# Performance work log

Measured on AMD Instinct MI355X. Metric: run time of the kernel, lower is better.

Reference implementation:

```python
import jax, jax.numpy as jnp
import numpy as np

K_STEPS = 10
ALPHA = 0.1


def setup_inputs() -> dict:
    key = jax.random.key(0)
    k0, k1, k2, k3 = jax.random.split(key, 4)
    N, E, C_IN, C_HID, C_OUT = 100000, 3200000, 512, 256, 64
    x = jax.random.normal(k0, (N, C_IN), dtype=jnp.float32)
    edge_index = jax.random.randint(k1, (2, E), 0, N, dtype=jnp.int64)
    W1 = jax.random.normal(k2, (C_IN, C_HID), dtype=jnp.float32) * (1.0 / np.sqrt(C_IN))
    b1 = jnp.zeros((C_HID,), dtype=jnp.float32)
    W2 = jax.random.normal(k3, (C_HID, C_OUT), dtype=jnp.float32) * (1.0 / np.sqrt(C_HID))
    b2 = jnp.zeros((C_OUT,), dtype=jnp.float32)
    return {"x": x, "edge_index": edge_index, "W1": W1, "b1": b1, "W2": W2, "b2": b2}


def reference(x, edge_index, W1, b1, W2, b2):
    N = x.shape[0]
    src, dst = edge_index[0], edge_index[1]
    # add self-loops (PyG APPNP default)
    loop = jnp.arange(N, dtype=src.dtype)
    src = jnp.concatenate([src, loop])
    dst = jnp.concatenate([dst, loop])
    # GCN symmetric normalization: D^{-1/2} A D^{-1/2}
    deg = jax.ops.segment_sum(jnp.ones_like(dst, dtype=x.dtype), dst, num_segments=N)
    dinv = jnp.where(deg > 0, deg ** -0.5, jnp.zeros_like(deg))
    norm = dinv[src] * dinv[dst]  # [E+N]
    # MLP (dropout is identity at inference)
    h = jax.nn.relu(x @ W1 + b1) @ W2 + b2  # [N, C_OUT]
    # K-step APPNP propagation with teleport
    out = h
    for _ in range(K_STEPS):
        msg = norm[:, None] * out[src]  # [E+N, C_OUT]
        agg = jax.ops.segment_sum(msg, dst, num_segments=N)
        out = (1.0 - ALPHA) * agg + ALPHA * h
    return jax.nn.log_softmax(out, axis=1)
```

## Files before the change

### kernel.cpp

```cpp
#include <hip/hip_runtime.h>
#include <hip/hip_bf16.h>

#define C_IN  512
#define C_HID 256
#define C_OUT 64
#define K_STEPS 10
#define ALPHA 0.1f

#define BKT_SHIFT 9
#define BKT_NODES 512
#define BCAP 24576
#define EPB 4096

typedef _Float16 half8 __attribute__((ext_vector_type(8)));
typedef float f32x4 __attribute__((ext_vector_type(4)));


__global__ __launch_bounds__(256) void k_bucketA(
    const int* __restrict__ src, const int* __restrict__ dst, int E,
    int* __restrict__ bcursor, long long* __restrict__ bedges, int nbkt)
{
    __shared__ int lcount[256];
    __shared__ int lbase[256];
    int t = threadIdx.x;
    int base = blockIdx.x * EPB;
    for (int i = t; i < nbkt; i += 256) lcount[i] = 0;
    __syncthreads();

    int       mybkt[16];
    int       myoff[16];
    long long mypk[16];
    #pragma unroll
    for (int j = 0; j < 16; j++) {
        int e = base + j * 256 + t;
        if (e < E) {
            int s = src[e], d = dst[e];
            int b = d >> BKT_SHIFT;
            mybkt[j] = b;
            mypk[j]  = ((long long)d << 32) | (unsigned int)s;
            myoff[j] = atomicAdd(&lcount[b], 1);
        } else {
            mybkt[j] = -1;
        }
    }
    __syncthreads();
    for (int i = t; i < nbkt; i += 256)
        lbase[i] = lcount[i] ? atomicAdd(&bcursor[i], lcount[i]) : 0;
    __syncthreads();
    #pragma unroll
    for (int j = 0; j < 16; j++) {
        if (mybkt[j] >= 0) {
            int p = lbase[mybkt[j]] + myoff[j];
            bedges[(size_t)mybkt[j] * BCAP + p] = mypk[j];
        }
    }
}

__global__ __launch_bounds__(256) void k_bcount(
    const int* __restrict__ bcursor, const long long* __restrict__ bedges,
    int* __restrict__ counts, int N)
{
    __shared__ int lcnt[BKT_NODES];
    int b = blockIdx.x, t = threadIdx.x;
    int nodebase = b << BKT_SHIFT;
    for (int i = t; i < BKT_NODES; i += 256) lcnt[i] = 0;
    __syncthreads();
    int cnt = bcursor[b];
    const long long* be = bedges + (size_t)b * BCAP;
    for (int i = t; i < cnt; i += 256) {
        int d = (int)(be[i] >> 32);
        atomicAdd(&lcnt[d - nodebase], 1);
    }
    __syncthreads();
    for (int i = t; i < BKT_NODES; i += 256) {
        int node = nodebase + i;
        if (node < N) counts[node] = lcnt[i];
    }
}

__global__ __launch_bounds__(256) void k_bscatter(
    const int* __restrict__ bcursor, const long long* __restrict__ bedges,
    const int* __restrict__ rowptr, int* __restrict__ csr_src, int N)
{
    __shared__ int lcur[BKT_NODES];
    int b = blockIdx.x, t = threadIdx.x;
    int nodebase = b << BKT_SHIFT;
    for (int i = t; i < BKT_NODES; i += 256) {
        int node = nodebase + i;
        lcur[i] = (node < N) ? rowptr[node] : 0;
    }
    __syncthreads();
    int cnt = bcursor[b];
    const long long* be = bedges + (size_t)b * BCAP;
    for (int i = t; i < cnt; i += 256) {
        long long pk = be[i];
        int d = (int)(pk >> 32);
        int s = (int)pk;
        int p = atomicAdd(&lcur[d - nodebase], 1);
        csr_src[p] = s;
    }
}


__global__ void k_dinv(const int* __restrict__ counts, float* __restrict__ dinv, int N) {
    int i = blockIdx.x * blockDim.x + threadIdx.x;
    if (i < N) {
        float deg = (float)(counts[i] + 1);
        dinv[i] = 1.0f / sqrtf(deg);
    }
}

#define SCAN_CHUNK 2048

__global__ void k_scan1(const int* __restrict__ counts, int N, int* __restrict__ bsum) {
    __shared__ int sdata[256];
    int b = blockIdx.x, t = threadIdx.x;
    int base = b * SCAN_CHUNK;
    int sum = 0;
    for (int i = t; i < SCAN_CHUNK; i += 256) {
        int idx = base + i;
        sum += (idx < N) ? counts[idx] : 0;
    }
    sdata[t] = sum;
    __syncthreads();
    for (int off = 128; off; off >>= 1) {
        if (t < off) sdata[t] += sdata[t + off];
        __syncthreads();
    }
    if (t == 0) bsum[b] = sdata[0];
}

__global__ void k_scan2(int* __restrict__ bsum, int nb, int E, int* __restrict__ rowptr, int N) {
    if (blockIdx.x == 0 && threadIdx.x == 0) {
        int run = 0;
        for (int i = 0; i < nb; i++) { int v = bsum[i]; bsum[i] = run; run += v; }
        rowptr[N] = E;
    }
}

__global__ void k_scan3(const int* __restrict__ counts, int N,
                        const int* __restrict__ bsum, int* __restrict__ rowptr) {
    __shared__ int sdata[256];
    int b = blockIdx.x, t = threadIdx.x;
    int base = b * SCAN_CHUNK;
    int vals[8];
    int local = 0;
    #pragma unroll
    for (int i = 0; i < 8; i++) {
        int idx = base + t * 8 + i;
        vals[i] = (idx < N) ? counts[idx] : 0;
        local += vals[i];
    }
    sdata[t] = local;
    __syncthreads();
    for (int off = 1; off < 256; off <<= 1) {
        int y = 0;
        if (t >= off) y = sdata[t - off];
        __syncthreads();
        sdata[t] += y;
        __syncthreads();
    }
    int excl = (t == 0) ? 0 : sdata[t - 1];
    int run = bsum[b] + excl;
    #pragma unroll
    for (int i = 0; i < 8; i++) {
        int idx = base + t * 8 + i;
        if (idx < N) rowptr[idx] = run;
        run += vals[i];
    }
}


__global__ void k_w1t(const float* __restrict__ W, _Float16* __restrict__ Wt) {
    int i = blockIdx.x * 256 + threadIdx.x;
    int k = i >> 8, n = i & 255;
    Wt[(size_t)n * 512 + k] = (_Float16)W[i];
}

__global__ void k_w2t(const float* __restrict__ W, _Float16* __restrict__ Wt) {
    int i = blockIdx.x * 256 + threadIdx.x;
    int k = i >> 6, n = i & 63;
    Wt[(size_t)n * 256 + k] = (_Float16)W[i];
}


__global__ __launch_bounds__(256, 2) void k_mlp1(
    const float* __restrict__ A, const _Float16* __restrict__ Bt,
    const float* __restrict__ bias, _Float16* __restrict__ C, int M)
{
    __shared__ float lds[3][128 * 32];

    int t    = threadIdx.x;
    int lane = t & 63;
    int wid  = t >> 6;
    int bm   = blockIdx.x * 128;
    int wr   = wid >> 1;
    int wc   = wid & 1;
    int mrow = lane & 15;
    int kg   = lane >> 4;

    int srow = wid * 8 + (lane >> 3);
    int cgs  = (lane & 7) ^ (lane >> 3);

    const float* gsrc[4];
    #pragma unroll
    for (int q = 0; q < 4; q++) {
        int gr = bm + q * 32 + srow;
        if (gr >= M) gr = M - 1;
        gsrc[q] = A + (size_t)gr * 512 + cgs * 4;
    }

    #define STAGE(buf, ks)                                                       \
        {                                                                        \
            _Pragma("unroll")                                                    \
            for (int q = 0; q < 4; q++) {                                        \
                __builtin_amdgcn_global_load_lds(                                \
                    (const __attribute__((address_space(1))) void*)(gsrc[q] + (ks) * 32), \
                    (__attribute__((address_space(3))) void*)((char*)&lds[buf][0] + q * 4096 + wid * 1024), \
                    16, 0, 0);                                                   \
            }                                                                    \
        }

    f32x4 acc[4][8] = {};

    int m7 = lane & 7;
    int rbase[4];
    #pragma unroll
    for (int mi = 0; mi < 4; mi++)
        rbase[mi] = (wr * 64 + mi * 16 + mrow) * 32;
    int p0 = ((2 * kg) ^ m7) * 4;
    int p1 = ((2 * kg + 1) ^ m7) * 4;

    STAGE(0, 0);
    STAGE(1, 1);

    #pragma unroll
    for (int ks = 0; ks < 16; ks++) {
        asm volatile("s_waitcnt vmcnt(4) lgkmcnt(0)" ::: "memory");
        __builtin_amdgcn_s_barrier();

        half8 b[8];
        #pragma unroll
        for (int ni = 0; ni < 8; ni++) {
            int n = wc * 128 + ni * 16 + mrow;
            b[ni] = *(const half8*)(Bt + (size_t)n * 512 + ks * 32 + kg * 8);
        }

        if (ks < 14) STAGE((ks + 2) % 3, ks + 2);

        const float* lbuf = &lds[ks % 3][0];

        half8 a[4];
        #pragma unroll
        for (int mi = 0; mi < 4; mi++) {
            f32x4 lo = *(const f32x4*)&lbuf[rbase[mi] + p0];
            f32x4 hi = *(const f32x4*)&lbuf[rbase[mi] + p1];
            a[mi][0] = (_Float16)lo[0]; a[mi][1] = (_Float16)lo[1];
            a[mi][2] = (_Float16)lo[2]; a[mi][3] = (_Float16)lo[3];
            a[mi][4] = (_Float16)hi[0]; a[mi][5] = (_Float16)hi[1];
            a[mi][6] = (_Float16)hi[2]; a[mi][7] = (_Float16)hi[3];
        }

        #pragma unroll
        for (int mi = 0; mi < 4; mi++)
            #pragma unroll
            for (int ni = 0; ni < 8; ni++)
                acc[mi][ni] = __builtin_amdgcn_mfma_f32_16x16x32_f16(
                    a[mi], b[ni], acc[mi][ni], 0, 0, 0);
    }
    #undef STAGE

    #pragma unroll
    for (int mi = 0; mi < 4; mi++) {
        #pragma unroll
        for (int ni = 0; ni < 8; ni++) {
            int n = wc * 128 + ni * 16 + mrow;
            float bv = bias[n];
            #pragma unroll
            for (int rg = 0; rg < 4; rg++) {
                int row = bm + wr * 64 + mi * 16 + kg * 4 + rg;
                if (row < M) {
                    float v = acc[mi][ni][rg] + bv;
                    C[(size_t)row * 256 + n] = (_Float16)fmaxf(v, 0.f);
                }
            }
        }
    }
}


__global__ __launch_bounds__(256) void k_mlp2(
    const _Float16* __restrict__ A, const _Float16* __restrict__ Bt,
    const float* __restrict__ bias, const float* __restrict__ dinv,
    _Float16* __restrict__ C, _Float16* __restrict__ Y, int M)
{
    int lane = threadIdx.x & 63;
    int wid  = threadIdx.x >> 6;
    int bm   = blockIdx.x * 256 + wid * 64;
    int mrow = lane & 15;
    int kg   = lane >> 4;
    f32x4 acc[4][4] = {};

    int r[4];
    #pragma unroll
    for (int mi = 0; mi < 4; mi++) {
        int rr = bm + mi * 16 + mrow;
        r[mi] = rr < M ? rr : M - 1;
    }

    for (int k0 = 0; k0 < 256; k0 += 32) {
        int k = k0 + kg * 8;
        half8 a[4], b[4];
        #pragma unroll
        for (int mi = 0; mi < 4; mi++)
            a[mi] = *(const half8*)(A + (size_t)r[mi] * 256 + k);
        #pragma unroll
        for (int ni = 0; ni < 4; ni++) {
            int n = ni * 16 + mrow;
            b[ni] = *(const half8*)(Bt + (size_t)n * 256 + k);
        }
        #pragma unroll
        for (int mi = 0; mi < 4; mi++)
            #pragma unroll
            for (int ni = 0; ni < 4; ni++)
                acc[mi][ni] = __builtin_amdgcn_mfma_f32_16x16x32_f16(
                    a[mi], b[ni], acc[mi][ni], 0, 0, 0);
    }

    #pragma unroll
    for (int mi = 0; mi < 4; mi++) {
        #pragma unroll
        for (int ni = 0; ni < 4; ni++) {
            int n = ni * 16 + mrow;
            float bv = bias[n];
            #pragma unroll
            for (int rg = 0; rg < 4; rg++) {
                int row = bm + mi * 16 + kg * 4 + rg;
                if (row < M) {
                    float v = acc[mi][ni][rg] + bv;
                    C[(size_t)row * 64 + n] = (_Float16)v;
                    Y[(size_t)row * 64 + n] = (_Float16)(v * dinv[row]);
                }
            }
        }
    }
}


template <bool LAST>
__global__ __launch_bounds__(256) void k_prop(
    const int* __restrict__ rowptr, const int* __restrict__ csr_src,
    const float* __restrict__ dinv, const _Float16* __restrict__ h,
    const _Float16* __restrict__ ycur, _Float16* __restrict__ ynxt,
    float* __restrict__ out, int N)
{
    int node = blockIdx.x * 4 + (threadIdx.x >> 6);
    if (node >= N) return;
    int lane = threadIdx.x & 63;
    int g  = lane >> 3;
    int cg = lane & 7;

    int beg = rowptr[node], end = rowptr[node + 1];
    float dn = dinv[node];
    half8 ys = *(const half8*)(ycur + ((size_t)node << 6) + cg * 8);
    half8 hv = *(const half8*)(h    + ((size_t)node << 6) + cg * 8);

    float acc[8] = {};
    for (int e = beg + g; e < end; e += 32) {
        int i1 = e + 8, i2 = e + 16, i3 = e + 24;
        float p1 = (i1 < end) ? 1.f : 0.f;
        float p2 = (i2 < end) ? 1.f : 0.f;
        float p3 = (i3 < end) ? 1.f : 0.f;
        int s0 = csr_src[e];
        int s1 = csr_src[(i1 < end) ? i1 : e];
        int s2 = csr_src[(i2 < end) ? i2 : e];
        int s3 = csr_src[(i3 < end) ? i3 : e];
        half8 v0 = *(const half8*)(ycur + ((size_t)s0 << 6) + cg * 8);
        half8 v1 = *(const half8*)(ycur + ((size_t)s1 << 6) + cg * 8);
        half8 v2 = *(const half8*)(ycur + ((size_t)s2 << 6) + cg * 8);
        half8 v3 = *(const half8*)(ycur + ((size_t)s3 << 6) + cg * 8);
        #pragma unroll
        for (int c = 0; c < 8; c++)
            acc[c] += ((float)v0[c] + p1 * (float)v1[c])
                    + (p2 * (float)v2[c] + p3 * (float)v3[c]);
    }

    #pragma unroll
    for (int c = 0; c < 8; c++) {
        float a = acc[c];
        a += __shfl_xor(a, 8);
        a += __shfl_xor(a, 16);
        a += __shfl_xor(a, 32);
        acc[c] = a;
    }

    float o[8];
    #pragma unroll
    for (int c = 0; c < 8; c++)
        o[c] = (1.0f - ALPHA) * dn * (acc[c] + (float)ys[c]) + ALPHA * (float)hv[c];

    if (!LAST) {
        if (g == 0) {
            half8 w;
            #pragma unroll
            for (int c = 0; c < 8; c++) w[c] = (_Float16)(dn * o[c]);
            *(half8*)(ynxt + ((size_t)node << 6) + cg * 8) = w;
        }
    } else {
        float m = o[0];
        #pragma unroll
        for (int c = 1; c < 8; c++) m = fmaxf(m, o[c]);
        m = fmaxf(m, __shfl_xor(m, 1));
        m = fmaxf(m, __shfl_xor(m, 2));
        m = fmaxf(m, __shfl_xor(m, 4));
        float s = 0.f;
        #pragma unroll
        for (int c = 0; c < 8; c++) s += __expf(o[c] - m);
        s += __shfl_xor(s, 1);
        s += __shfl_xor(s, 2);
        s += __shfl_xor(s, 4);
        float ls = m + logf(s);
        if (g == 0) {
            f32x4 w0, w1;
            #pragma unroll
            for (int c = 0; c < 4; c++) { w0[c] = o[c] - ls; w1[c] = o[c + 4] - ls; }
            float* p = out + ((size_t)node << 6) + cg * 8;
            *(f32x4*)p = w0;
            *(f32x4*)(p + 4) = w1;
        }
    }
}


extern "C" void kernel_launch(void* const* d_in, const int* in_sizes, int n_in,
                              void* d_out, int out_size, void* d_ws, size_t ws_size,
                              hipStream_t stream) {
    const float* x  = (const float*)d_in[0];
    const int*   ei = (const int*)d_in[1];
    const float* W1 = (const float*)d_in[2];
    const float* b1 = (const float*)d_in[3];
    const float* W2 = (const float*)d_in[4];
    const float* b2 = (const float*)d_in[5];

    const int N = in_sizes[0] / C_IN;
    const int E = in_sizes[1] / 2;
    const int* src = ei;
    const int* dst = ei + E;

    char* ws = (char*)d_ws;
    size_t off = 0;
    auto alloc = [&](size_t bytes) -> void* {
        void* p = ws + off;
        off += (bytes + 255) & ~(size_t)255;
        return p;
    };

    int nb   = (N + SCAN_CHUNK - 1) / SCAN_CHUNK;
    int nbkt = (N + BKT_NODES - 1) / BKT_NODES;

    int*       counts  = (int*)      alloc((size_t)4 * N);
    int*       rowptr  = (int*)      alloc((size_t)4 * (N + 1));
    float*     dinv    = (float*)    alloc((size_t)4 * N);
    int*       bsum    = (int*)      alloc((size_t)4 * (nb + 1));
    int*       bcursor = (int*)      alloc((size_t)4 * nbkt);
    int*       csr_src = (int*)      alloc((size_t)4 * E);
    _Float16*  W1t     = (_Float16*) alloc((size_t)2 * C_IN * C_HID);
    _Float16*  W2t     = (_Float16*) alloc((size_t)2 * C_HID * C_OUT);
    _Float16*  hmid    = (_Float16*) alloc((size_t)2 * N * C_HID);
    _Float16*  h       = (_Float16*) alloc((size_t)2 * N * C_OUT);
    _Float16*  ybuf0   = (_Float16*) alloc((size_t)2 * N * C_OUT);
    _Float16*  ybuf1   = (_Float16*) alloc((size_t)2 * N * C_OUT);
    _Float16*  ybuf2   = (_Float16*) alloc((size_t)2 * N * C_OUT);

    long long* bedges = (long long*)hmid;

    hipMemsetAsync(bcursor, 0, (size_t)4 * nbkt, stream);
    k_bucketA<<<(E + EPB - 1) / EPB, 256, 0, stream>>>(src, dst, E, bcursor, bedges, nbkt);
    k_bcount<<<nbkt, 256, 0, stream>>>(bcursor, bedges, counts, N);
    k_dinv<<<(N + 255) / 256, 256, 0, stream>>>(counts, dinv, N);
    k_scan1<<<nb, 256, 0, stream>>>(counts, N, bsum);
    k_scan2<<<1, 64, 0, stream>>>(bsum, nb, E, rowptr, N);
    k_scan3<<<nb, 256, 0, stream>>>(counts, N, bsum, rowptr);
    k_bscatter<<<nbkt, 256, 0, stream>>>(bcursor, bedges, rowptr, csr_src, N);

    k_w1t<<<(C_IN * C_HID) / 256, 256, 0, stream>>>(W1, W1t);
    k_w2t<<<(C_HID * C_OUT) / 256, 256, 0, stream>>>(W2, W2t);
    k_mlp1<<<(N + 127) / 128, 256, 0, stream>>>(x, W1t, b1, hmid, N);
    k_mlp2<<<(N + 255) / 256, 256, 0, stream>>>(hmid, W2t, b2, dinv, h, ybuf0, N);

    int pgrid = (N + 3) / 4;
    _Float16* ycur = ybuf0;
    for (int it = 0; it < K_STEPS - 1; ++it) {
        _Float16* ynxt = (it & 1) ? ybuf2 : ybuf1;
        k_prop<false><<<pgrid, 256, 0, stream>>>(rowptr, csr_src, dinv, h, ycur, ynxt, nullptr, N);
        ycur = ynxt;
    }
    k_prop<true><<<pgrid, 256, 0, stream>>>(rowptr, csr_src, dinv, h, ycur, nullptr, (float*)d_out, N);
}
```

Baseline: 773.2 us.

## Fuse CSR build kernels per bucket and simplify MLP1 pipelining

```diff
diff --git a/kernel.cpp b/kernel.cpp
--- a/kernel.cpp
+++ b/kernel.cpp
@@ -56,15 +56,31 @@
     }
 }
 
-__global__ __launch_bounds__(256) void k_bcount(
-    const int* __restrict__ bcursor, const long long* __restrict__ bedges,
-    int* __restrict__ counts, int N)
+__global__ void k_bscan(const int* __restrict__ bcursor, int nbkt,
+                        int* __restrict__ bktbase, int* __restrict__ rowptr,
+                        int N, int E)
+{
+    if (blockIdx.x == 0 && threadIdx.x == 0) {
+        int run = 0;
+        for (int i = 0; i < nbkt; i++) { bktbase[i] = run; run += bcursor[i]; }
+        rowptr[N] = E;
+    }
+}
+
+__global__ __launch_bounds__(256) void k_bfin(
+    const int* __restrict__ bcursor, const int* __restrict__ bktbase,
+    const long long* __restrict__ bedges, int* __restrict__ rowptr,
+    float* __restrict__ dinv, int* __restrict__ csr_src, int N)
 {
     __shared__ int lcnt[BKT_NODES];
+    __shared__ int lofs[BKT_NODES];
+    __shared__ int sdata[256];
     int b = blockIdx.x, t = threadIdx.x;
     int nodebase = b << BKT_SHIFT;
-    for (int i = t; i < BKT_NODES; i += 256) lcnt[i] = 0;
-    __syncthreads();
+
+    lcnt[2 * t] = 0; lcnt[2 * t + 1] = 0;
+    __syncthreads();
+
     int cnt = bcursor[b];
     const long long* be = bedges + (size_t)b * BCAP;
     for (int i = t; i < cnt; i += 256) {
@@ -72,86 +88,10 @@
         atomicAdd(&lcnt[d - nodebase], 1);
     }
     __syncthreads();
-    for (int i = t; i < BKT_NODES; i += 256) {
-        int node = nodebase + i;
-        if (node < N) counts[node] = lcnt[i];
-    }
-}
-
-__global__ __launch_bounds__(256) void k_bscatter(
-    const int* __restrict__ bcursor, const long long* __restrict__ bedges,
-    const int* __restrict__ rowptr, int* __restrict__ csr_src, int N)
-{
-    __shared__ int lcur[BKT_NODES];
-    int b = blockIdx.x, t = threadIdx.x;
-    int nodebase = b << BKT_SHIFT;
-    for (int i = t; i < BKT_NODES; i += 256) {
-        int node = nodebase + i;
-        lcur[i] = (node < N) ? rowptr[node] : 0;
-    }
-    __syncthreads();
-    int cnt = bcursor[b];
-    const long long* be = bedges + (size_t)b * BCAP;
-    for (int i = t; i < cnt; i += 256) {
-        long long pk = be[i];
-        int d = (int)(pk >> 32);
-        int s = (int)pk;
-        int p = atomicAdd(&lcur[d - nodebase], 1);
-        csr_src[p] = s;
-    }
-}
-
-
-__global__ void k_dinv(const int* __restrict__ counts, float* __restrict__ dinv, int N) {
-    int i = blockIdx.x * blockDim.x + threadIdx.x;
-    if (i < N) {
-        float deg = (float)(counts[i] + 1);
-        dinv[i] = 1.0f / sqrtf(deg);
-    }
-}
-
-#define SCAN_CHUNK 2048
-
-__global__ void k_scan1(const int* __restrict__ counts, int N, int* __restrict__ bsum) {
-    __shared__ int sdata[256];
-    int b = blockIdx.x, t = threadIdx.x;
-    int base = b * SCAN_CHUNK;
-    int sum = 0;
-    for (int i = t; i < SCAN_CHUNK; i += 256) {
-        int idx = base + i;
-        sum += (idx < N) ? counts[idx] : 0;
-    }
-    sdata[t] = sum;
-    __syncthreads();
-    for (int off = 128; off; off >>= 1) {
-        if (t < off) sdata[t] += sdata[t + off];
-        __syncthreads();
-    }
-    if (t == 0) bsum[b] = sdata[0];
-}
-
-__global__ void k_scan2(int* __restrict__ bsum, int nb, int E, int* __restrict__ rowptr, int N) {
-    if (blockIdx.x == 0 && threadIdx.x == 0) {
-        int run = 0;
-        for (int i = 0; i < nb; i++) { int v = bsum[i]; bsum[i] = run; run += v; }
-        rowptr[N] = E;
-    }
-}
-
-__global__ void k_scan3(const int* __restrict__ counts, int N,
-                        const int* __restrict__ bsum, int* __restrict__ rowptr) {
-    __shared__ int sdata[256];
-    int b = blockIdx.x, t = threadIdx.x;
-    int base = b * SCAN_CHUNK;
-    int vals[8];
-    int local = 0;
-    #pragma unroll
-    for (int i = 0; i < 8; i++) {
-        int idx = base + t * 8 + i;
-        vals[i] = (idx < N) ? counts[idx] : 0;
-        local += vals[i];
-    }
-    sdata[t] = local;
+
+    int v0 = lcnt[2 * t], v1 = lcnt[2 * t + 1];
+    int psum = v0 + v1;
+    sdata[t] = psum;
     __syncthreads();
     for (int off = 1; off < 256; off <<= 1) {
         int y = 0;
@@ -160,27 +100,47 @@
         sdata[t] += y;
         __syncthreads();
     }
-    int excl = (t == 0) ? 0 : sdata[t - 1];
-    int run = bsum[b] + excl;
-    #pragma unroll
-    for (int i = 0; i < 8; i++) {
-        int idx = base + t * 8 + i;
-        if (idx < N) rowptr[idx] = run;
-        run += vals[i];
-    }
-}
-
-
-__global__ void k_w1t(const float* __restrict__ W, _Float16* __restrict__ Wt) {
+    int excl = sdata[t] - psum;
+    int base = bktbase[b];
+    lofs[2 * t]     = base + excl;
+    lofs[2 * t + 1] = base + excl + v0;
+    __syncthreads();
+
+    #pragma unroll
+    for (int j = 0; j < 2; j++) {
+        int i = 2 * t + j;
+        int node = nodebase + i;
+        if (node < N) {
+            rowptr[node] = lofs[i];
+            dinv[node] = 1.0f / sqrtf((float)(lcnt[i] + 1));
+        }
+    }
+    __syncthreads();
+
+    for (int i = t; i < cnt; i += 256) {
+        long long pk = be[i];
+        int d = (int)(pk >> 32);
+        int s = (int)pk;
+        int p = atomicAdd(&lofs[d - nodebase], 1);
+        csr_src[p] = s;
+    }
+}
+
+
+__global__ void k_wt(const float* __restrict__ W1, const float* __restrict__ W2,
+                     _Float16* __restrict__ W1t, _Float16* __restrict__ W2t)
+{
     int i = blockIdx.x * 256 + threadIdx.x;
-    int k = i >> 8, n = i & 255;
-    Wt[(size_t)n * 512 + k] = (_Float16)W[i];
-}
-
-__global__ void k_w2t(const float* __restrict__ W, _Float16* __restrict__ Wt) {
-    int i = blockIdx.x * 256 + threadIdx.x;
-    int k = i >> 6, n = i & 63;
-    Wt[(size_t)n * 256 + k] = (_Float16)W[i];
+    if (i < C_IN * C_HID) {
+        int k = i >> 8, n = i & 255;
+        W1t[(size_t)n * 512 + k] = (_Float16)W1[i];
+    } else {
+        int j = i - C_IN * C_HID;
+        if (j < C_HID * C_OUT) {
+            int k = j >> 6, n = j & 63;
+            W2t[(size_t)n * 256 + k] = (_Float16)W2[j];
+        }
+    }
 }
 
 
@@ -188,7 +148,7 @@
     const float* __restrict__ A, const _Float16* __restrict__ Bt,
     const float* __restrict__ bias, _Float16* __restrict__ C, int M)
 {
-    __shared__ float lds[3][128 * 32];
+    __shared__ float lds[2][128 * 32];
 
     int t    = threadIdx.x;
     int lane = t & 63;
@@ -232,12 +192,11 @@
     int p1 = ((2 * kg + 1) ^ m7) * 4;
 
     STAGE(0, 0);
-    STAGE(1, 1);
-
-    #pragma unroll
+    __syncthreads();
+
+    int cur = 0;
     for (int ks = 0; ks < 16; ks++) {
-        asm volatile("s_waitcnt vmcnt(4) lgkmcnt(0)" ::: "memory");
-        __builtin_amdgcn_s_barrier();
+        if (ks < 15) STAGE(cur ^ 1, ks + 1);
 
         half8 b[8];
         #pragma unroll
@@ -246,15 +205,11 @@
             b[ni] = *(const half8*)(Bt + (size_t)n * 512 + ks * 32 + kg * 8);
         }
 
-        if (ks < 14) STAGE((ks + 2) % 3, ks + 2);
-
-        const float* lbuf = &lds[ks % 3][0];
-
         half8 a[4];
         #pragma unroll
         for (int mi = 0; mi < 4; mi++) {
-            f32x4 lo = *(const f32x4*)&lbuf[rbase[mi] + p0];
-            f32x4 hi = *(const f32x4*)&lbuf[rbase[mi] + p1];
+            f32x4 lo = *(const f32x4*)&lds[cur][rbase[mi] + p0];
+            f32x4 hi = *(const f32x4*)&lds[cur][rbase[mi] + p1];
             a[mi][0] = (_Float16)lo[0]; a[mi][1] = (_Float16)lo[1];
             a[mi][2] = (_Float16)lo[2]; a[mi][3] = (_Float16)lo[3];
             a[mi][4] = (_Float16)hi[0]; a[mi][5] = (_Float16)hi[1];
@@ -267,6 +222,9 @@
             for (int ni = 0; ni < 8; ni++)
                 acc[mi][ni] = __builtin_amdgcn_mfma_f32_16x16x32_f16(
                     a[mi], b[ni], acc[mi][ni], 0, 0, 0);
+
+        __syncthreads();
+        cur ^= 1;
     }
     #undef STAGE
 
@@ -455,14 +413,12 @@
         return p;
     };
 
-    int nb   = (N + SCAN_CHUNK - 1) / SCAN_CHUNK;
     int nbkt = (N + BKT_NODES - 1) / BKT_NODES;
 
-    int*       counts  = (int*)      alloc((size_t)4 * N);
     int*       rowptr  = (int*)      alloc((size_t)4 * (N + 1));
     float*     dinv    = (float*)    alloc((size_t)4 * N);
-    int*       bsum    = (int*)      alloc((size_t)4 * (nb + 1));
     int*       bcursor = (int*)      alloc((size_t)4 * nbkt);
+    int*       bktbase = (int*)      alloc((size_t)4 * (nbkt + 1));
     int*       csr_src = (int*)      alloc((size_t)4 * E);
     _Float16*  W1t     = (_Float16*) alloc((size_t)2 * C_IN * C_HID);
     _Float16*  W2t     = (_Float16*) alloc((size_t)2 * C_HID * C_OUT);
@@ -476,15 +432,11 @@
 
     hipMemsetAsync(bcursor, 0, (size_t)4 * nbkt, stream);
     k_bucketA<<<(E + EPB - 1) / EPB, 256, 0, stream>>>(src, dst, E, bcursor, bedges, nbkt);
-    k_bcount<<<nbkt, 256, 0, stream>>>(bcursor, bedges, counts, N);
-    k_dinv<<<(N + 255) / 256, 256, 0, stream>>>(counts, dinv, N);
-    k_scan1<<<nb, 256, 0, stream>>>(counts, N, bsum);
-    k_scan2<<<1, 64, 0, stream>>>(bsum, nb, E, rowptr, N);
-    k_scan3<<<nb, 256, 0, stream>>>(counts, N, bsum, rowptr);
-    k_bscatter<<<nbkt, 256, 0, stream>>>(bcursor, bedges, rowptr, csr_src, N);
-
-    k_w1t<<<(C_IN * C_HID) / 256, 256, 0, stream>>>(W1, W1t);
-    k_w2t<<<(C_HID * C_OUT) / 256, 256, 0, stream>>>(W2, W2t);
+    k_bscan<<<1, 64, 0, stream>>>(bcursor, nbkt, bktbase, rowptr, N, E);
+    k_bfin<<<nbkt, 256, 0, stream>>>(bcursor, bktbase, bedges, rowptr, dinv, csr_src, N);
+
+    int wtot = C_IN * C_HID + C_HID * C_OUT;
+    k_wt<<<(wtot + 255) / 256, 256, 0, stream>>>(W1, W2, W1t, W2t);
     k_mlp1<<<(N + 127) / 128, 256, 0, stream>>>(x, W1t, b1, hmid, N);
     k_mlp2<<<(N + 255) / 256, 256, 0, stream>>>(hmid, W2t, b2, dinv, h, ybuf0, N);
 
```

Result: no change. 758.8 us (-1.9%).
